# Kernel tuning notes

Measured on AMD Instinct MI355X. Metric: run time of the kernel, lower is better.

Reference implementation:

```python
import jax, jax.numpy as jnp
import numpy as np

SIZE = 1024
CODE_DIM = 256

def setup_inputs() -> dict:
    key = jax.random.key(0)
    k1, k2 = jax.random.split(key)
    z = jax.random.normal(k1, (32, CODE_DIM, 32, 32), dtype=jnp.float32)
    # nn.Embedding weight init: uniform(-1/size, 1/size)
    emb_weight = jax.random.uniform(k2, (SIZE, CODE_DIM), dtype=jnp.float32,
                                    minval=-1.0 / SIZE, maxval=1.0 / SIZE)
    return {"z": z, "emb_weight": emb_weight}

def reference(z, emb_weight):
    n, c, h, w = z.shape
    # [n, h, w, c] -> [n*h*w, c]
    z_ = jnp.transpose(z, (0, 2, 3, 1)).reshape(-1, c)
    # squared euclidean distances to all codes: ||z||^2 - 2 z.W^T + ||W||^2
    distances = (jnp.sum(z_ ** 2, axis=1, keepdims=True)
                 - 2.0 * jnp.matmul(z_, emb_weight.T)
                 + jnp.sum(emb_weight ** 2, axis=1)[None, :])
    encoding_indices = jnp.argmin(distances, axis=1).reshape(n, h, w)
    # gather codes and move channel back: [n, h, w, c] -> [n, c, h, w]
    quantized = jnp.transpose(emb_weight[encoding_indices], (0, 3, 1, 2))
    straight_through = jax.lax.stop_gradient(quantized - z) + z
    return (quantized, straight_through, encoding_indices)
```

## Files before the change

### kernel.cpp

```cpp
#include <hip/hip_runtime.h>
#include <cfloat>


#define P_TOTAL   32768
#define N_CODES   1024
#define Q_ELEMS   8388608
#define EPS_SCREEN 4.0e-3f
#define CAND_CAP  128

typedef __attribute__((ext_vector_type(8))) short bf16x8;
typedef __attribute__((ext_vector_type(4))) float f32x4;

#define GLOAD16(gsrc, ldst) \
  __builtin_amdgcn_global_load_lds((const __attribute__((address_space(1))) void*)(gsrc), \
                                   (__attribute__((address_space(3))) void*)(ldst), 16, 0, 0)

__device__ __forceinline__ unsigned short f2bf(float f) {
    unsigned u = __builtin_bit_cast(unsigned, f);
    u += 0x7FFF + ((u >> 16) & 1);
    return (unsigned short)(u >> 16);
}

__device__ __forceinline__ float sq_sep(float v) {
    float t = v * v;
    asm volatile("" : "+v"(t));
    return t;
}

__global__ void k0t_transpose(const float* __restrict__ wemb, float* __restrict__ wt) {
    __shared__ float tile[64 * 65];
    const int tid = threadIdx.x;
    const int ct = blockIdx.x >> 2, kt = blockIdx.x & 3;
    const int c0 = ct * 64, k0 = kt * 64;
    const int rr = tid >> 4, cg = tid & 15;
    #pragma unroll
    for (int i = 0; i < 4; ++i) {
        const int row = i * 16 + rr;
        const float4 v = *(const float4*)&wemb[(size_t)(c0 + row) * 256 + k0 + cg * 4];
        tile[row * 65 + cg * 4 + 0] = v.x;
        tile[row * 65 + cg * 4 + 1] = v.y;
        tile[row * 65 + cg * 4 + 2] = v.z;
        tile[row * 65 + cg * 4 + 3] = v.w;
    }
    __syncthreads();
    #pragma unroll
    for (int i = 0; i < 4; ++i) {
        const int krow = i * 16 + rr;
        float4 v;
        v.x = tile[(cg * 4 + 0) * 65 + krow];
        v.y = tile[(cg * 4 + 1) * 65 + krow];
        v.z = tile[(cg * 4 + 2) * 65 + krow];
        v.w = tile[(cg * 4 + 3) * 65 + krow];
        *(float4*)&wt[(size_t)(k0 + krow) * 1024 + c0 + cg * 4] = v;
    }
}

__global__ void k0w_pack(const float* __restrict__ wemb, unsigned short* __restrict__ whi) {
    const int t = blockIdx.x * 256 + threadIdx.x;
    const int c = t >> 5, g = t & 31;
    const float4 v0 = *(const float4*)&wemb[(size_t)c * 256 + g * 8];
    const float4 v1 = *(const float4*)&wemb[(size_t)c * 256 + g * 8 + 4];
    bf16x8 hv;
    hv[0] = (short)f2bf(v0.x); hv[1] = (short)f2bf(v0.y);
    hv[2] = (short)f2bf(v0.z); hv[3] = (short)f2bf(v0.w);
    hv[4] = (short)f2bf(v1.x); hv[5] = (short)f2bf(v1.y);
    hv[6] = (short)f2bf(v1.z); hv[7] = (short)f2bf(v1.w);
    const int gs = g ^ (c & 7);
    *(bf16x8*)(whi + (size_t)c * 256 + gs * 8) = hv;
}

#define T16S 280
__global__ void k0z_pack(const float* __restrict__ z, unsigned short* __restrict__ zhi) {
    __shared__ unsigned short t16[64 * T16S];
    const int tid = threadIdx.x;
    const int n = blockIdx.x >> 4, hc = blockIdx.x & 15;
    const int hw0 = hc * 64;
    const int w = tid >> 6, hl = tid & 63;
    #pragma unroll
    for (int i = 0; i < 64; ++i) {
        const int k = i * 4 + w;
        const float v = z[((size_t)(n * 256 + k) << 10) + hw0 + hl];
        t16[hl * T16S + k] = f2bf(v);
    }
    __syncthreads();
    const int row = tid >> 2, cp = tid & 3;
    const size_t p0 = (size_t)(n * 1024 + hw0);
    #pragma unroll
    for (int i = 0; i < 8; ++i) {
        const int chunk = i * 4 + cp;
        *(bf16x8*)(zhi + (p0 + row) * 256 + chunk * 8) =
            *(const bf16x8*)&t16[row * T16S + chunk * 8];
    }
}

__global__ void k1_wsq(const float* __restrict__ wemb, float* __restrict__ wsq,
                       int* __restrict__ candCnt) {
    const int b = blockIdx.x, tid = threadIdx.x;
    if (b >= 4) { candCnt[(b - 4) * 256 + tid] = 0; return; }
    const int c = b * 256 + tid;
    const float* base = wemb + (size_t)c * 256;
    float half[2];
    #pragma unroll
    for (int h = 0; h < 2; ++h) {
        const float* x = base + h * 128;
        float r[8];
        #pragma unroll
        for (int j = 0; j < 8; ++j) r[j] = sq_sep(x[j]);
        for (int i = 8; i < 128; i += 8) {
            #pragma unroll
            for (int j = 0; j < 8; ++j) r[j] += sq_sep(x[i + j]);
        }
        half[h] = ((r[0] + r[1]) + (r[2] + r[3])) + ((r[4] + r[5]) + (r[6] + r[7]));
    }
    wsq[c] = half[0] + half[1];
}

__launch_bounds__(256, 4)
__global__ void k2s_screen(const unsigned short* __restrict__ zhi,
                           const unsigned short* __restrict__ whi,
                           const float* __restrict__ wsq,
                           unsigned short* __restrict__ candC,
                           int* __restrict__ candCnt) {
    __shared__ unsigned short Bs[2][32 * 256];
    const int tid = threadIdx.x, bid = blockIdx.x;
    const int pgrp = bid >> 1, half = bid & 1;
    const int w = tid >> 6, l = tid & 63;
    const int la = l & 15, kg = l >> 4;
    const int m0 = pgrp * 64 + w * 16;
    const int cb0 = half * 512;

    bf16x8 af[8];
    #pragma unroll
    for (int ks = 0; ks < 8; ++ks)
        af[ks] = *(const bf16x8*)(zhi + (size_t)(m0 + la) * 256 + ks * 32 + kg * 8);

    float rg[4];
    #pragma unroll
    for (int r = 0; r < 4; ++r) rg[r] = FLT_MAX;

#define STAGEB(buf, cb_) do {                                                  \
    const unsigned short* src_ = whi + (size_t)(cb_) * 256;                    \
    _Pragma("unroll")                                                          \
    for (int i_ = 0; i_ < 4; ++i_)                                             \
        GLOAD16(src_ + i_ * 2048 + tid * 8, &Bs[buf][i_ * 2048 + tid * 8]);    \
} while (0)

    STAGEB(0, cb0);
    __syncthreads();

    for (int ch = 0; ch < 16; ++ch) {
        const int cur = ch & 1;
        const int cb = cb0 + ch * 32;
        if (ch < 15) STAGEB(cur ^ 1, cb + 32);

        float wsqv[2];
        #pragma unroll
        for (int nf = 0; nf < 2; ++nf) wsqv[nf] = wsq[cb + nf * 16 + la];

        f32x4 acc[2];
        #pragma unroll
        for (int nf = 0; nf < 2; ++nf) acc[nf] = (f32x4){0.f, 0.f, 0.f, 0.f};

        #pragma unroll
        for (int ks = 0; ks < 8; ++ks) {
            bf16x8 bfv[2];
            #pragma unroll
            for (int nf = 0; nf < 2; ++nf) {
                const int cl = nf * 16 + la;
                const int slot = (ks * 4 + kg) ^ (cl & 7);
                bfv[nf] = *(const bf16x8*)&Bs[cur][cl * 256 + slot * 8];
            }
            #pragma unroll
            for (int nf = 0; nf < 2; ++nf)
                acc[nf] = __builtin_amdgcn_mfma_f32_16x16x32_bf16(
                    af[ks], bfv[nf], acc[nf], 0, 0, 0);
        }

        float da[2][4];
        #pragma unroll
        for (int nf = 0; nf < 2; ++nf)
            #pragma unroll
            for (int r = 0; r < 4; ++r)
                da[nf][r] = __builtin_fmaf(-2.f, acc[nf][r], wsqv[nf]);

        #pragma unroll
        for (int r = 0; r < 4; ++r) {
            float mv = fminf(da[0][r], da[1][r]);
            #pragma unroll
            for (int off = 1; off < 16; off <<= 1)
                mv = fminf(mv, __shfl_xor(mv, off));
            rg[r] = fminf(rg[r], mv);
        }

        #pragma unroll
        for (int nf = 0; nf < 2; ++nf)
            #pragma unroll
            for (int r = 0; r < 4; ++r)
                if (da[nf][r] <= rg[r] + EPS_SCREEN) {
                    const int p = pgrp * 64 + w * 16 + kg * 4 + r;
                    const int slot = atomicAdd(&candCnt[p], 1);
                    if (slot < CAND_CAP)
                        candC[(size_t)p * CAND_CAP + slot] =
                            (unsigned short)(cb + nf * 16 + la);
                }

        __syncthreads();
    }
#undef STAGEB
}

__launch_bounds__(256, 4)
__global__ void k2r_rescore(const float* __restrict__ z, const float* __restrict__ wemb,
                            const float* __restrict__ wsq,
                            const unsigned short* __restrict__ candC,
                            const int* __restrict__ candCnt,
                            float* __restrict__ idx_out) {
    __shared__ float t32[32 * 256];
    const int tid = threadIdx.x;
    const int wv = tid >> 6, l = tid & 63;
    const int p0 = blockIdx.x * 32;
    const int n = p0 >> 10, hw0 = p0 & 1023;

    const int pl = tid >> 3, slot = tid & 7;
    const int p = p0 + pl;
    const int count = candCnt[p];
    const int c0 = candC[(size_t)p * CAND_CAP + slot];

    const int row = l & 31;
    const int xmr = (row & 7) * 4;
    #pragma unroll
    for (int i = 0; i < 8; ++i) {
        const int k4 = i * 32 + wv * 8 + (l >> 5) * 4;
        const size_t zb = ((size_t)(n * 256 + k4) << 10) + hw0 + row;
        float4 v;
        v.x = z[zb];
        v.y = z[zb + 1024];
        v.z = z[zb + 2048];
        v.w = z[zb + 3072];
        *(float4*)&t32[row * 256 + (k4 ^ xmr)] = v;
    }
    __syncthreads();

    const float* zrow = &t32[pl * 256];
    const int xm = (pl & 7) * 4;

    float halfv[2];
    #pragma unroll
    for (int h = 0; h < 2; ++h) {
        float r[8];
        {
            const f32x4 a = *(const f32x4*)&zrow[(h * 128) ^ xm];
            const f32x4 b = *(const f32x4*)&zrow[(h * 128 + 4) ^ xm];
            #pragma unroll
            for (int j = 0; j < 4; ++j) { r[j] = sq_sep(a[j]); r[4 + j] = sq_sep(b[j]); }
        }
        for (int i = 8; i < 128; i += 8) {
            const f32x4 a = *(const f32x4*)&zrow[(h * 128 + i) ^ xm];
            const f32x4 b = *(const f32x4*)&zrow[(h * 128 + i + 4) ^ xm];
            #pragma unroll
            for (int j = 0; j < 4; ++j) { r[j] += sq_sep(a[j]); r[4 + j] += sq_sep(b[j]); }
        }
        halfv[h] = ((r[0] + r[1]) + (r[2] + r[3])) + ((r[4] + r[5]) + (r[6] + r[7]));
    }
    const float zsv = halfv[0] + halfv[1];

#define DOT_CHAIN(wb_, dot_) do {                                              \
    _Pragma("unroll")                                                          \
    for (int kb = 0; kb < 256; kb += 8) {                                      \
        const f32x4 za = *(const f32x4*)&zrow[kb ^ xm];                        \
        const f32x4 zb4 = *(const f32x4*)&zrow[(kb + 4) ^ xm];                 \
        const float4 wa = *(const float4*)&(wb_)[kb];                          \
        const float4 wc = *(const float4*)&(wb_)[kb + 4];                      \
        dot_ = __builtin_fmaf(za[0], wa.x, dot_);                              \
        dot_ = __builtin_fmaf(za[1], wa.y, dot_);                              \
        dot_ = __builtin_fmaf(za[2], wa.z, dot_);                              \
        dot_ = __builtin_fmaf(za[3], wa.w, dot_);                              \
        dot_ = __builtin_fmaf(zb4[0], wc.x, dot_);                             \
        dot_ = __builtin_fmaf(zb4[1], wc.y, dot_);                             \
        dot_ = __builtin_fmaf(zb4[2], wc.z, dot_);                             \
        dot_ = __builtin_fmaf(zb4[3], wc.w, dot_);                             \
    }                                                                          \
} while (0)

    float bd = FLT_MAX;
    int bc = N_CODES;

    if (count <= CAND_CAP) {
        const int nr = (count + 7) >> 3;
        for (int rr = 0; rr < nr; ++rr) {
            const int s = rr * 8 + slot;
            if (s < count) {
                const int c = (rr == 0) ? c0 : candC[(size_t)p * CAND_CAP + s];
                const float* wb = wemb + (size_t)c * 256;
                float dot = 0.f;
                DOT_CHAIN(wb, dot);
                const float d = __builtin_fmaf(-2.f, dot, zsv) + wsq[c];
                if (d < bd || (d == bd && c < bc)) { bd = d; bc = c; }
            }
        }
    } else {
        for (int rr = 0; rr < 128; ++rr) {
            const int c = rr * 8 + slot;
            const float* wb = wemb + (size_t)c * 256;
            float dot = 0.f;
            DOT_CHAIN(wb, dot);
            const float d = __builtin_fmaf(-2.f, dot, zsv) + wsq[c];
            if (d < bd || (d == bd && c < bc)) { bd = d; bc = c; }
        }
    }
#undef DOT_CHAIN

    #pragma unroll
    for (int off = 1; off < 8; off <<= 1) {
        const float od = __shfl_xor(bd, off);
        const int   oi = __shfl_xor(bc, off);
        if (od < bd || (od == bd && oi < bc)) { bd = od; bc = oi; }
    }
    if (slot == 0) idx_out[p] = (float)bc;
}

__global__ void k3_gather(const float* __restrict__ z, const float* __restrict__ wtf,
                          const float* __restrict__ idxf,
                          float* __restrict__ out0, float* __restrict__ out1) {
    __shared__ float wcol[1024];
    const int tid = threadIdx.x;
    const int b = blockIdx.x;
    const int c = b & 255, n = b >> 8;
    *(float4*)&wcol[tid * 4] = *(const float4*)&wtf[(size_t)c * 1024 + tid * 4];
    __syncthreads();

    const size_t zo = (((size_t)(n * 256 + c)) << 10) + tid * 4;
    const float4 zv = *(const float4*)&z[zo];
    const float4 iv = *(const float4*)&idxf[n * 1024 + tid * 4];
    float4 qv, st;
    qv.x = wcol[(int)iv.x]; st.x = (qv.x - zv.x) + zv.x;
    qv.y = wcol[(int)iv.y]; st.y = (qv.y - zv.y) + zv.y;
    qv.z = wcol[(int)iv.z]; st.z = (qv.z - zv.z) + zv.z;
    qv.w = wcol[(int)iv.w]; st.w = (qv.w - zv.w) + zv.w;
    *(float4*)&out0[zo] = qv;
    *(float4*)&out1[zo] = st;
}

extern "C" void kernel_launch(void* const* d_in, const int* in_sizes, int n_in,
                              void* d_out, int out_size, void* d_ws, size_t ws_size,
                              hipStream_t stream) {
    const float* z = (const float*)d_in[0];
    const float* wemb = (const float*)d_in[1];
    float* out = (float*)d_out;
    float* out0 = out;
    float* out1 = out + Q_ELEMS;
    float* oidx = out + 2 * Q_ELEMS;
    unsigned short* zhi = (unsigned short*)out0;
    unsigned short* candC = (unsigned short*)(out0 + 4194304);
    int* candCnt = (int*)(out0 + 6291456);
    unsigned short* whi = (unsigned short*)out1;
    float* wsq = (float*)d_ws;
    float* wtf = (float*)d_ws + 1024;

    k0t_transpose<<<64, 256, 0, stream>>>(wemb, wtf);
    k0w_pack<<<128, 256, 0, stream>>>(wemb, whi);
    k0z_pack<<<512, 256, 0, stream>>>(z, zhi);
    k1_wsq<<<132, 256, 0, stream>>>(wemb, wsq, candCnt);
    k2s_screen<<<1024, 256, 0, stream>>>(zhi, whi, wsq, candC, candCnt);
    k2r_rescore<<<P_TOTAL / 32, 256, 0, stream>>>(z, wemb, wsq, candC, candCnt, oidx);
    k3_gather<<<8192, 256, 0, stream>>>(z, wtf, oidx, out0, out1);
}
```

Baseline: 192.8 us.

## Store screen distances and prune rescore candidates against the final approximate minimum

The screening kernel now records each candidate's approximate bf16 distance next to its code index. The rescore kernel takes the per-point minimum of those distances and keeps only candidates within EPS of it. When exactly one candidate survives it writes that index directly and the block skips the exact fp32 dot products. The candidate cap is halved to 64, which adds more overflow cases that fall back to a full scan, and the extra distance buffer costs additional global writes and reads.

```diff
diff --git a/kernel.cpp b/kernel.cpp
--- a/kernel.cpp
+++ b/kernel.cpp
@@ -6,7 +6,7 @@
 #define N_CODES   1024
 #define Q_ELEMS   8388608
 #define EPS_SCREEN 4.0e-3f
-#define CAND_CAP  128
+#define CAND_CAP  64
 
 typedef __attribute__((ext_vector_type(8))) short bf16x8;
 typedef __attribute__((ext_vector_type(4))) float f32x4;
@@ -120,6 +120,7 @@
                            const unsigned short* __restrict__ whi,
                            const float* __restrict__ wsq,
                            unsigned short* __restrict__ candC,
+                           float* __restrict__ candD,
                            int* __restrict__ candCnt) {
     __shared__ unsigned short Bs[2][32 * 256];
     const int tid = threadIdx.x, bid = blockIdx.x;
@@ -199,9 +200,11 @@
                 if (da[nf][r] <= rg[r] + EPS_SCREEN) {
                     const int p = pgrp * 64 + w * 16 + kg * 4 + r;
                     const int slot = atomicAdd(&candCnt[p], 1);
-                    if (slot < CAND_CAP)
+                    if (slot < CAND_CAP) {
                         candC[(size_t)p * CAND_CAP + slot] =
                             (unsigned short)(cb + nf * 16 + la);
+                        candD[(size_t)p * CAND_CAP + slot] = da[nf][r];
+                    }
                 }
 
         __syncthreads();
@@ -213,6 +216,7 @@
 __global__ void k2r_rescore(const float* __restrict__ z, const float* __restrict__ wemb,
                             const float* __restrict__ wsq,
                             const unsigned short* __restrict__ candC,
+                            const float* __restrict__ candD,
                             const int* __restrict__ candCnt,
                             float* __restrict__ idx_out) {
     __shared__ float t32[32 * 256];
@@ -224,7 +228,8 @@
     const int pl = tid >> 3, slot = tid & 7;
     const int p = p0 + pl;
     const int count = candCnt[p];
-    const int c0 = candC[(size_t)p * CAND_CAP + slot];
+    const int c0raw = candC[(size_t)p * CAND_CAP + slot];
+    const float da0 = candD[(size_t)p * CAND_CAP + slot];
 
     const int row = l & 31;
     const int xmr = (row & 7) * 4;
@@ -239,7 +244,47 @@
         v.w = z[zb + 3072];
         *(float4*)&t32[row * 256 + (k4 ^ xmr)] = v;
     }
+
+    bool need;
+    float thr = 0.f;
+    if (count <= CAND_CAP) {
+        const int nr = (count + 7) >> 3;
+        float m = (slot < count) ? da0 : FLT_MAX;
+        for (int rr = 1; rr < nr; ++rr) {
+            const int s = rr * 8 + slot;
+            if (s < count) m = fminf(m, candD[(size_t)p * CAND_CAP + s]);
+        }
+        #pragma unroll
+        for (int off = 1; off < 8; off <<= 1) m = fminf(m, __shfl_xor(m, off));
+        thr = m + EPS_SCREEN;
+
+        int V;
+        int soleC = N_CODES;
+        {
+            const bool v0 = (slot < count) && (da0 <= thr);
+            const unsigned long long mask = __ballot(v0);
+            V = __popcll((mask >> ((l >> 3) * 8)) & 0xFFull);
+            if (v0) soleC = c0raw;
+        }
+        for (int rr = 1; rr < nr; ++rr) {
+            const int s = rr * 8 + slot;
+            bool vs = false;
+            if (s < count) {
+                vs = (candD[(size_t)p * CAND_CAP + s] <= thr);
+                if (vs && soleC == N_CODES) soleC = candC[(size_t)p * CAND_CAP + s];
+            }
+            const unsigned long long mask = __ballot(vs);
+            V += __popcll((mask >> ((l >> 3) * 8)) & 0xFFull);
+        }
+        if (V == 1 && soleC != N_CODES) idx_out[p] = (float)soleC;
+        need = (V >= 2);
+    } else {
+        need = true;
+    }
+
     __syncthreads();
+
+    if (!need) return;
 
     const float* zrow = &t32[pl * 256];
     const int xm = (pl & 7) * 4;
@@ -289,8 +334,13 @@
         const int nr = (count + 7) >> 3;
         for (int rr = 0; rr < nr; ++rr) {
             const int s = rr * 8 + slot;
-            if (s < count) {
-                const int c = (rr == 0) ? c0 : candC[(size_t)p * CAND_CAP + s];
+            int c; float das;
+            if (rr == 0) { c = c0raw; das = da0; }
+            else if (s < count) {
+                c = candC[(size_t)p * CAND_CAP + s];
+                das = candD[(size_t)p * CAND_CAP + s];
+            } else { c = N_CODES; das = FLT_MAX; }
+            if (s < count && das <= thr) {
                 const float* wb = wemb + (size_t)c * 256;
                 float dot = 0.f;
                 DOT_CHAIN(wb, dot);
@@ -352,7 +402,8 @@
     float* oidx = out + 2 * Q_ELEMS;
     unsigned short* zhi = (unsigned short*)out0;
     unsigned short* candC = (unsigned short*)(out0 + 4194304);
-    int* candCnt = (int*)(out0 + 6291456);
+    float* candD = out0 + 5242880;
+    int* candCnt = (int*)(out0 + 7340032);
     unsigned short* whi = (unsigned short*)out1;
     float* wsq = (float*)d_ws;
     float* wtf = (float*)d_ws + 1024;
@@ -361,7 +412,7 @@
     k0w_pack<<<128, 256, 0, stream>>>(wemb, whi);
     k0z_pack<<<512, 256, 0, stream>>>(z, zhi);
     k1_wsq<<<132, 256, 0, stream>>>(wemb, wsq, candCnt);
-    k2s_screen<<<1024, 256, 0, stream>>>(zhi, whi, wsq, candC, candCnt);
-    k2r_rescore<<<P_TOTAL / 32, 256, 0, stream>>>(z, wemb, wsq, candC, candCnt, oidx);
+    k2s_screen<<<1024, 256, 0, stream>>>(zhi, whi, wsq, candC, candD, candCnt);
+    k2r_rescore<<<P_TOTAL / 32, 256, 0, stream>>>(z, wemb, wsq, candC, candD, candCnt, oidx);
     k3_gather<<<8192, 256, 0, stream>>>(z, wtf, oidx, out0, out1);
 }
```

After: 167.0 us. -13.4%, faster.
